# Kernel optimization log

Hardware: AMD Instinct MI355X
Metric: run time of the kernel (lower is better)

## Reference

```python
import jax, jax.numpy as jnp
import numpy as np

NEG_SLOPE = 0.01  # nn.LeakyReLU default


def setup_inputs() -> dict:
    key = jax.random.key(0)
    k1, k2, k3, k4, k5 = jax.random.split(key, 5)
    SLI, FEAT, NODE = 8, 64, 20000
    N = SLI * NODE          # 160000 graph nodes
    E = 2_560_000           # avg degree 16
    OUT = 64
    inputs = jax.random.normal(k1, (SLI, FEAT, NODE), dtype=jnp.float32)
    src = jax.random.randint(k2, (E,), 0, N, dtype=jnp.int64)
    dst = jax.random.randint(k3, (E,), 0, N, dtype=jnp.int64)
    # GraphConv params (glorot-ish scale)
    W = jax.random.normal(k4, (FEAT, OUT), dtype=jnp.float32) / np.sqrt(FEAT)
    b = jnp.zeros((OUT,), dtype=jnp.float32)
    return {"inputs": inputs, "W": W, "b": b, "src": src, "dst": dst}


def reference(inputs, W, b, src, dst):
    # inputs: [sli, feat, node] -> [sli*node, feat]  (dropout is eval-mode identity)
    sli, feat, node = inputs.shape
    x = jnp.transpose(inputs, (0, 2, 1)).reshape(-1, feat)
    N = sli * node
    ones = jnp.ones(src.shape, dtype=x.dtype)
    deg_out = jax.ops.segment_sum(ones, src, num_segments=N)  # out-degree of src
    deg_in = jax.ops.segment_sum(ones, dst, num_segments=N)   # in-degree of dst
    norm_src = jnp.where(deg_out > 0, deg_out, 1.0) ** -0.5
    norm_dst = jnp.where(deg_in > 0, deg_in, 1.0) ** -0.5
    # norm='both': scale src feats, sum-aggregate over edges, scale dst
    h = x * norm_src[:, None]
    agg = jax.ops.segment_sum(h[src], dst, num_segments=N)    # [N, feat]
    agg = agg * norm_dst[:, None]
    out = agg @ W + b                                          # [N, out]
    out = jax.nn.leaky_relu(out, NEG_SLOPE)
    # [N, out] -> [sli, node, out] -> [sli, out, node]
    return jnp.transpose(out.reshape(sli, node, -1), (0, 2, 1))
```

## Files before the change

kernel.cpp:

```cpp
#include <hip/hip_runtime.h>
#include <hip/hip_bf16.h>

constexpr int SLI  = 8;
constexpr int FEAT = 64;
constexpr int NODE = 20000;
constexpr int NTOT = SLI * NODE;
constexpr int OUTF = 64;
constexpr int CAP  = 48;
constexpr int NBD  = 625;
constexpr int NBS  = 313;
constexpr int BCAPD = 4864;
constexpr int BCAPS = 8960;
constexpr int EPB  = 4096;
constexpr int NDST = NTOT / 256;

typedef __attribute__((ext_vector_type(8))) short bf16x8;
typedef __attribute__((ext_vector_type(4))) float f32x4;

static __device__ inline unsigned short f2bf(float x) {
    unsigned u = __float_as_uint(x);
    unsigned r = (u + 0x7fffu + ((u >> 16) & 1u)) >> 16;
    return (unsigned short)r;
}

__global__ __launch_bounds__(256) void k_part(const int* __restrict__ src,
                                              const int* __restrict__ dst,
                                              int* __restrict__ cursor_d,
                                              unsigned* __restrict__ bucket_d,
                                              int* __restrict__ cursor_s,
                                              unsigned short* __restrict__ bucket_s, int E) {
    __shared__ unsigned       svalD[EPB];
    __shared__ unsigned short sbktD[EPB];
    __shared__ unsigned sS[EPB];
    __shared__ int histD[NBD], loffD[NBD], lcurD[NBD], baseD[NBD];
    __shared__ int histS[NBS], loffS[NBS], lcurS[NBS], baseS[NBS];
    __shared__ int goffD[64], goffS[64];
    int t  = threadIdx.x;
    int e0 = blockIdx.x * EPB;
    for (int i = t; i < NBD; i += 256) histD[i] = 0;
    for (int i = t; i < NBS; i += 256) histS[i] = 0;
    __syncthreads();
    int myS[16], myD[16];
#pragma unroll
    for (int i = 0; i < 4; ++i) {
        int j  = (e0 >> 2) + i * 256 + t;
        int b4 = j << 2;
        if (b4 + 3 < E) {
            int4 vs = ((const int4*)src)[j];
            int4 vd = ((const int4*)dst)[j];
            myS[4*i+0] = vs.x; myS[4*i+1] = vs.y; myS[4*i+2] = vs.z; myS[4*i+3] = vs.w;
            myD[4*i+0] = vd.x; myD[4*i+1] = vd.y; myD[4*i+2] = vd.z; myD[4*i+3] = vd.w;
        } else {
#pragma unroll
            for (int c = 0; c < 4; ++c) {
                int idx = b4 + c;
                myS[4*i+c] = (idx < E) ? src[idx] : -1;
                myD[4*i+c] = (idx < E) ? dst[idx] : -1;
            }
        }
    }
#pragma unroll
    for (int i = 0; i < 16; ++i) {
        if (myD[i] >= 0) {
            atomicAdd(&histD[myD[i] >> 8], 1);
            atomicAdd(&histS[myS[i] >> 9], 1);
        }
    }
    __syncthreads();
    int wv = t >> 6, ln = t & 63;
    if (wv == 0) {
        int b0 = ln * 10, s = 0;
#pragma unroll
        for (int j = 0; j < 10; ++j) { int bb = b0 + j; if (bb < NBD) s += histD[bb]; }
        int x = s;
        for (int off = 1; off < 64; off <<= 1) {
            int y = __shfl_up(x, off, 64);
            if (ln >= off) x += y;
        }
        goffD[ln] = x - s;
    } else if (wv == 1) {
        int b0 = ln * 5, s = 0;
#pragma unroll
        for (int j = 0; j < 5; ++j) { int bb = b0 + j; if (bb < NBS) s += histS[bb]; }
        int x = s;
        for (int off = 1; off < 64; off <<= 1) {
            int y = __shfl_up(x, off, 64);
            if (ln >= off) x += y;
        }
        goffS[ln] = x - s;
    }
    __syncthreads();
    for (int bb = t; bb < NBD; bb += 256) {
        int g = bb / 10;
        int sD = goffD[g];
        for (int k = g * 10; k < bb; ++k) sD += histD[k];
        loffD[bb] = sD; lcurD[bb] = sD;
        baseD[bb] = atomicAdd(&cursor_d[bb], histD[bb]);
    }
    for (int bb = t; bb < NBS; bb += 256) {
        int g = bb / 5;
        int sS2 = goffS[g];
        for (int k = g * 5; k < bb; ++k) sS2 += histS[k];
        loffS[bb] = sS2; lcurS[bb] = sS2;
        baseS[bb] = atomicAdd(&cursor_s[bb], histS[bb]);
    }
    __syncthreads();
#pragma unroll
    for (int i = 0; i < 16; ++i) {
        if (myD[i] >= 0) {
            int bD = myD[i] >> 8;
            int p  = atomicAdd(&lcurD[bD], 1);
            svalD[p] = ((unsigned)(myD[i] & 255) << 18) | (unsigned)myS[i];
            sbktD[p] = (unsigned short)bD;
            int bS = myS[i] >> 9;
            int q  = atomicAdd(&lcurS[bS], 1);
            sS[q] = ((unsigned)bS << 9) | (unsigned)(myS[i] & 511);
        }
    }
    __syncthreads();
    int nval = E - e0; if (nval > EPB) nval = EPB;
    for (int p = t; p < nval; p += 256) {
        int bD = sbktD[p];
        int wi = baseD[bD] + (p - loffD[bD]);
        if (wi < BCAPD) bucket_d[(size_t)bD * BCAPD + wi] = svalD[p];
        unsigned vs = sS[p];
        int bS = vs >> 9;
        int wj = baseS[bS] + (p - loffS[bS]);
        if (wj < BCAPS) bucket_s[(size_t)bS * BCAPS + wj] = (unsigned short)(vs & 511);
    }
}

__global__ __launch_bounds__(256) void k_fin(const int* __restrict__ cursor_d,
                                             const unsigned* __restrict__ bucket_d,
                                             const int* __restrict__ cursor_s,
                                             const unsigned short* __restrict__ bucket_s,
                                             int* __restrict__ col_ell,
                                             int* __restrict__ deg_in,
                                             int* __restrict__ deg_out) {
    __shared__ char lds[256 * CAP * 4 + 2048];
    int t = threadIdx.x;
    if (blockIdx.x < NDST) {
        int* ell = (int*)lds;
        int* cnt = (int*)(lds + 256 * CAP * 4);
        int b = blockIdx.x;
        cnt[t] = 0;
        __syncthreads();
        int len = cursor_d[b]; if (len > BCAPD) len = BCAPD;
        const unsigned* p = bucket_d + (size_t)b * BCAPD;
        for (int i = t; i < len; i += 256) {
            unsigned e = p[i];
            int r = (e >> 18) & 255;
            int pos = atomicAdd(&cnt[r], 1);
            if (pos < CAP) ell[r * CAP + pos] = (int)(e & 0x3FFFFu);
        }
        __syncthreads();
        int node0 = b << 8;
        deg_in[node0 + t] = cnt[t];
        size_t gbase = (size_t)node0 * CAP;
        const int4* lsrc = (const int4*)ell;
        int4* gdst = (int4*)(col_ell + gbase);
#pragma unroll
        for (int i = 0; i < 12; ++i)
            gdst[i * 256 + t] = lsrc[i * 256 + t];
    } else {
        int* cnt = (int*)lds;
        int b = blockIdx.x - NDST;
        cnt[t] = 0; cnt[t + 256] = 0;
        __syncthreads();
        int len = cursor_s[b]; if (len > BCAPS) len = BCAPS;
        const unsigned short* p = bucket_s + (size_t)b * BCAPS;
        for (int i = t; i < len; i += 256)
            atomicAdd(&cnt[p[i]], 1);
        __syncthreads();
        int n0 = b << 9;
        if (n0 + t < NTOT)       deg_out[n0 + t] = cnt[t];
        if (n0 + 256 + t < NTOT) deg_out[n0 + 256 + t] = cnt[t + 256];
    }
}

__global__ __launch_bounds__(256) void k_transpose(const float* __restrict__ in,
                                                   const int* __restrict__ deg_out,
                                                   unsigned short* __restrict__ xs) {
    __shared__ float tile[64][65];
    int sli = blockIdx.y;
    int n0  = blockIdx.x * 64;
    int t   = threadIdx.x;
    int fx  = t & 15;
    int fr  = t >> 4;
    const float* ip = in + (size_t)sli * FEAT * NODE;
    int nq = n0 + fx * 4;
#pragma unroll
    for (int i = 0; i < 4; ++i) {
        int f = fr + i * 16;
        float4 v = {0.f, 0.f, 0.f, 0.f};
        if (nq < NODE) v = *(const float4*)(ip + (size_t)f * NODE + nq);
        tile[f][fx * 4 + 0] = v.x;
        tile[f][fx * 4 + 1] = v.y;
        tile[f][fx * 4 + 2] = v.z;
        tile[f][fx * 4 + 3] = v.w;
    }
    __syncthreads();
    int h  = t & 31;
    int nr = t >> 5;
#pragma unroll
    for (int i = 0; i < 8; ++i) {
        int nl   = nr + i * 8;
        int node = n0 + nl;
        if (node < NODE) {
            int n = sli * NODE + node;
            int d = deg_out[n];
            float sc = rsqrtf(d > 0 ? (float)d : 1.f);
            unsigned lo = f2bf(tile[2 * h][nl] * sc);
            unsigned hi = f2bf(tile[2 * h + 1][nl] * sc);
            *(unsigned*)(xs + (size_t)n * 64 + 2 * h) = lo | (hi << 16);
        }
    }
}

__global__ __launch_bounds__(256) void k_agg_gemm(const int* __restrict__ deg_in,
                                                  const int* __restrict__ col_ell,
                                                  const unsigned short* __restrict__ xs,
                                                  const float* __restrict__ W,
                                                  const float* __restrict__ b,
                                                  float* __restrict__ out) {
    __shared__ char lds[18432];
    unsigned short* av = (unsigned short*)lds;
    unsigned short* wt = (unsigned short*)(lds + 9216);
    float (*otile)[65] = (float(*)[65])lds;

    int t    = threadIdx.x;
    int lane = t & 63;
    int w    = t >> 6;
    int g8   = lane >> 3;
    int f8   = lane & 7;
    int sli  = blockIdx.y;
    int n0   = blockIdx.x * 64;

#pragma unroll
    for (int i = 0; i < 16; ++i) {
        int idx = i * 256 + t;
        int f = idx >> 6, o = idx & 63;
        wt[o * 72 + f] = f2bf(W[idx]);
    }

    int m0 = w * 16;
    for (int ii = 0; ii < 16; ii += 2) {
        int rowA = m0 + ii, rowB = rowA + 1;
        int nodeA = n0 + rowA, nodeB = n0 + rowB;
        int nA = sli * NODE + nodeA, nB = sli * NODE + nodeB;
        int dA = (nodeA < NODE) ? deg_in[nA] : 0;
        int dB = (nodeB < NODE) ? deg_in[nB] : 0;
        int degA = dA < CAP ? dA : CAP;
        int degB = dB < CAP ? dB : CAP;
        int cA = (lane < degA) ? col_ell[(size_t)nA * CAP + lane] : NTOT;
        int cB = (lane < degB) ? col_ell[(size_t)nB * CAP + lane] : NTOT;
        float accA[8] = {0,0,0,0,0,0,0,0};
        float accB[8] = {0,0,0,0,0,0,0,0};
        int gmax = degA > degB ? degA : degB;
        int groups = (gmax + 7) >> 3;
#pragma unroll 2
        for (int j = 0; j < groups; ++j) {
            int idx = 8 * j + g8;
            int sA = __shfl(cA, idx, 64);
            int sB = __shfl(cB, idx, 64);
            uint4 vA = *(const uint4*)(xs + (size_t)sA * 64 + f8 * 8);
            uint4 vB = *(const uint4*)(xs + (size_t)sB * 64 + f8 * 8);
            accA[0] += __uint_as_float(vA.x << 16);
            accA[1] += __uint_as_float(vA.x & 0xffff0000u);
            accA[2] += __uint_as_float(vA.y << 16);
            accA[3] += __uint_as_float(vA.y & 0xffff0000u);
            accA[4] += __uint_as_float(vA.z << 16);
            accA[5] += __uint_as_float(vA.z & 0xffff0000u);
            accA[6] += __uint_as_float(vA.w << 16);
            accA[7] += __uint_as_float(vA.w & 0xffff0000u);
            accB[0] += __uint_as_float(vB.x << 16);
            accB[1] += __uint_as_float(vB.x & 0xffff0000u);
            accB[2] += __uint_as_float(vB.y << 16);
            accB[3] += __uint_as_float(vB.y & 0xffff0000u);
            accB[4] += __uint_as_float(vB.z << 16);
            accB[5] += __uint_as_float(vB.z & 0xffff0000u);
            accB[6] += __uint_as_float(vB.w << 16);
            accB[7] += __uint_as_float(vB.w & 0xffff0000u);
        }
#pragma unroll
        for (int k = 0; k < 8; ++k) {
            accA[k] += __shfl_xor(accA[k], 8, 64);
            accA[k] += __shfl_xor(accA[k], 16, 64);
            accA[k] += __shfl_xor(accA[k], 32, 64);
            accB[k] += __shfl_xor(accB[k], 8, 64);
            accB[k] += __shfl_xor(accB[k], 16, 64);
            accB[k] += __shfl_xor(accB[k], 32, 64);
        }
        if (g8 == 0) {
            float scA = rsqrtf(dA > 0 ? (float)dA : 1.f);
            float scB = rsqrtf(dB > 0 ? (float)dB : 1.f);
            uint4 hv;
            hv.x = (unsigned)f2bf(accA[0] * scA) | ((unsigned)f2bf(accA[1] * scA) << 16);
            hv.y = (unsigned)f2bf(accA[2] * scA) | ((unsigned)f2bf(accA[3] * scA) << 16);
            hv.z = (unsigned)f2bf(accA[4] * scA) | ((unsigned)f2bf(accA[5] * scA) << 16);
            hv.w = (unsigned)f2bf(accA[6] * scA) | ((unsigned)f2bf(accA[7] * scA) << 16);
            ((uint4*)(av + rowA * 72))[f8] = hv;
            hv.x = (unsigned)f2bf(accB[0] * scB) | ((unsigned)f2bf(accB[1] * scB) << 16);
            hv.y = (unsigned)f2bf(accB[2] * scB) | ((unsigned)f2bf(accB[3] * scB) << 16);
            hv.z = (unsigned)f2bf(accB[4] * scB) | ((unsigned)f2bf(accB[5] * scB) << 16);
            hv.w = (unsigned)f2bf(accB[6] * scB) | ((unsigned)f2bf(accB[7] * scB) << 16);
            ((uint4*)(av + rowB * 72))[f8] = hv;
        }
    }

    __syncthreads();

    int q = lane >> 4, r16 = lane & 15;
    bf16x8 afr[2], bfr[4][2];
#pragma unroll
    for (int ks = 0; ks < 2; ++ks)
        afr[ks] = *(const bf16x8*)(av + (m0 + r16) * 72 + ks * 32 + q * 8);
#pragma unroll
    for (int nt = 0; nt < 4; ++nt)
#pragma unroll
        for (int ks = 0; ks < 2; ++ks)
            bfr[nt][ks] = *(const bf16x8*)(wt + (nt * 16 + r16) * 72 + ks * 32 + q * 8);

    f32x4 acc4[4];
#pragma unroll
    for (int nt = 0; nt < 4; ++nt) acc4[nt] = (f32x4){0.f, 0.f, 0.f, 0.f};
#pragma unroll
    for (int nt = 0; nt < 4; ++nt)
#pragma unroll
        for (int ks = 0; ks < 2; ++ks)
            acc4[nt] = __builtin_amdgcn_mfma_f32_16x16x32_bf16(afr[ks], bfr[nt][ks], acc4[nt], 0, 0, 0);
    __syncthreads();

#pragma unroll
    for (int nt = 0; nt < 4; ++nt) {
        int oc = nt * 16 + r16;
        float bias = b[oc];
#pragma unroll
        for (int r = 0; r < 4; ++r) {
            float v = acc4[nt][r] + bias;
            v = v > 0.f ? v : 0.01f * v;
            otile[oc][m0 + q * 4 + r] = v;
        }
    }
    __syncthreads();

    const size_t obase = (size_t)sli * OUTF * NODE;
#pragma unroll
    for (int i = 0; i < 16; ++i) {
        int o    = w + i * 4;
        int node = n0 + lane;
        if (node < NODE)
            out[obase + (size_t)o * NODE + node] = otile[o][lane];
    }
}

extern "C" void kernel_launch(void* const* d_in, const int* in_sizes, int n_in,
                              void* d_out, int out_size, void* d_ws, size_t ws_size,
                              hipStream_t stream) {
    const float* inputs = (const float*)d_in[0];
    const float* W      = (const float*)d_in[1];
    const float* b      = (const float*)d_in[2];
    const int*   src    = (const int*)d_in[3];
    const int*   dst    = (const int*)d_in[4];
    float*       out    = (float*)d_out;
    const int E = in_sizes[3];

    char* ws = (char*)d_ws;
    int* deg_out = (int*)ws;
    int* deg_in  = (int*)(ws + (size_t)NTOT * 4);
    int* col_ell = (int*)(ws + (size_t)2 * NTOT * 4);
    char* R      = (char*)col_ell + (size_t)NTOT * CAP * 4;
    unsigned*       bucket_d = (unsigned*)R;
    unsigned short* bucket_s = (unsigned short*)(R + (size_t)NBD * BCAPD * 4);
    int*            cursors  = (int*)(R + (size_t)NBD * BCAPD * 4 + (size_t)NBS * BCAPS * 2);
    int* cursor_d = cursors;
    int* cursor_s = cursors + NBD;
    unsigned short* xs = (unsigned short*)R;

    hipMemsetAsync(cursors, 0, (size_t)(NBD + NBS) * 4, stream);
    hipMemsetAsync(xs + (size_t)NTOT * 64, 0, 64 * sizeof(unsigned short), stream);

    int PB = (E + EPB - 1) / EPB;
    k_part<<<PB, 256, 0, stream>>>(src, dst, cursor_d, bucket_d, cursor_s, bucket_s, E);

    k_fin<<<NDST + NBS, 256, 0, stream>>>(cursor_d, bucket_d, cursor_s, bucket_s,
                                          col_ell, deg_in, deg_out);

    dim3 tgrid((NODE + 63) / 64, SLI);
    k_transpose<<<tgrid, 256, 0, stream>>>(inputs, deg_out, xs);

    k_agg_gemm<<<tgrid, 256, 0, stream>>>(deg_in, col_ell, xs, W, b, out);
}
```

Baseline: 243.5 us.

## Issue partition cursor atomics early and widen finalize kernel to 512 threads

In the partition kernel, the global atomicAdd reservations on the bucket cursors now start right after the histogram, so their latency overlaps the in-block scan and scatter. Full __syncthreads are swapped for LDS-only waitcnt barriers, which do not wait on the pending global atomics. The loff arrays are dropped and recomputed as lcur minus hist, freeing LDS. The finalize kernel runs 512 threads per block for more parallelism per bucket, at the cost of more register pressure and reliance on hand-written barrier asm being correct.

Result: faster. 223.3 us (-8.3%).

```diff
diff --git a/kernel.cpp b/kernel.cpp
--- a/kernel.cpp
+++ b/kernel.cpp
@@ -32,8 +32,8 @@
     __shared__ unsigned       svalD[EPB];
     __shared__ unsigned short sbktD[EPB];
     __shared__ unsigned sS[EPB];
-    __shared__ int histD[NBD], loffD[NBD], lcurD[NBD], baseD[NBD];
-    __shared__ int histS[NBS], loffS[NBS], lcurS[NBS], baseS[NBS];
+    __shared__ int histD[NBD], lcurD[NBD], baseD[NBD];
+    __shared__ int histS[NBS], lcurS[NBS], baseS[NBS];
     __shared__ int goffD[64], goffS[64];
     int t  = threadIdx.x;
     int e0 = blockIdx.x * EPB;
@@ -67,6 +67,17 @@
         }
     }
     __syncthreads();
+    int rbD[3], rbS[2];
+#pragma unroll
+    for (int i = 0; i < 3; ++i) {
+        int bb = t + i * 256;
+        rbD[i] = (bb < NBD) ? atomicAdd(&cursor_d[bb], histD[bb]) : 0;
+    }
+#pragma unroll
+    for (int i = 0; i < 2; ++i) {
+        int bb = t + i * 256;
+        rbS[i] = (bb < NBS) ? atomicAdd(&cursor_s[bb], histS[bb]) : 0;
+    }
     int wv = t >> 6, ln = t & 63;
     if (wv == 0) {
         int b0 = ln * 10, s = 0;
@@ -89,22 +100,20 @@
         }
         goffS[ln] = x - s;
     }
-    __syncthreads();
+    asm volatile("s_waitcnt lgkmcnt(0)\n\ts_barrier" ::: "memory");
     for (int bb = t; bb < NBD; bb += 256) {
         int g = bb / 10;
         int sD = goffD[g];
         for (int k = g * 10; k < bb; ++k) sD += histD[k];
-        loffD[bb] = sD; lcurD[bb] = sD;
-        baseD[bb] = atomicAdd(&cursor_d[bb], histD[bb]);
+        lcurD[bb] = sD;
     }
     for (int bb = t; bb < NBS; bb += 256) {
         int g = bb / 5;
         int sS2 = goffS[g];
         for (int k = g * 5; k < bb; ++k) sS2 += histS[k];
-        loffS[bb] = sS2; lcurS[bb] = sS2;
-        baseS[bb] = atomicAdd(&cursor_s[bb], histS[bb]);
-    }
-    __syncthreads();
+        lcurS[bb] = sS2;
+    }
+    asm volatile("s_waitcnt lgkmcnt(0)\n\ts_barrier" ::: "memory");
 #pragma unroll
     for (int i = 0; i < 16; ++i) {
         if (myD[i] >= 0) {
@@ -117,20 +126,24 @@
             sS[q] = ((unsigned)bS << 9) | (unsigned)(myS[i] & 511);
         }
     }
+#pragma unroll
+    for (int i = 0; i < 3; ++i) { int bb = t + i * 256; if (bb < NBD) baseD[bb] = rbD[i]; }
+#pragma unroll
+    for (int i = 0; i < 2; ++i) { int bb = t + i * 256; if (bb < NBS) baseS[bb] = rbS[i]; }
     __syncthreads();
     int nval = E - e0; if (nval > EPB) nval = EPB;
     for (int p = t; p < nval; p += 256) {
         int bD = sbktD[p];
-        int wi = baseD[bD] + (p - loffD[bD]);
+        int wi = baseD[bD] + (p - (lcurD[bD] - histD[bD]));
         if (wi < BCAPD) bucket_d[(size_t)bD * BCAPD + wi] = svalD[p];
         unsigned vs = sS[p];
         int bS = vs >> 9;
-        int wj = baseS[bS] + (p - loffS[bS]);
+        int wj = baseS[bS] + (p - (lcurS[bS] - histS[bS]));
         if (wj < BCAPS) bucket_s[(size_t)bS * BCAPS + wj] = (unsigned short)(vs & 511);
     }
 }
 
-__global__ __launch_bounds__(256) void k_fin(const int* __restrict__ cursor_d,
+__global__ __launch_bounds__(512) void k_fin(const int* __restrict__ cursor_d,
                                              const unsigned* __restrict__ bucket_d,
                                              const int* __restrict__ cursor_s,
                                              const unsigned short* __restrict__ bucket_s,
@@ -143,11 +156,11 @@
         int* ell = (int*)lds;
         int* cnt = (int*)(lds + 256 * CAP * 4);
         int b = blockIdx.x;
-        cnt[t] = 0;
+        if (t < 256) cnt[t] = 0;
         __syncthreads();
         int len = cursor_d[b]; if (len > BCAPD) len = BCAPD;
         const unsigned* p = bucket_d + (size_t)b * BCAPD;
-        for (int i = t; i < len; i += 256) {
+        for (int i = t; i < len; i += 512) {
             unsigned e = p[i];
             int r = (e >> 18) & 255;
             int pos = atomicAdd(&cnt[r], 1);
@@ -155,26 +168,25 @@
         }
         __syncthreads();
         int node0 = b << 8;
-        deg_in[node0 + t] = cnt[t];
+        if (t < 256) deg_in[node0 + t] = cnt[t];
         size_t gbase = (size_t)node0 * CAP;
         const int4* lsrc = (const int4*)ell;
         int4* gdst = (int4*)(col_ell + gbase);
 #pragma unroll
-        for (int i = 0; i < 12; ++i)
-            gdst[i * 256 + t] = lsrc[i * 256 + t];
+        for (int i = 0; i < 6; ++i)
+            gdst[i * 512 + t] = lsrc[i * 512 + t];
     } else {
         int* cnt = (int*)lds;
         int b = blockIdx.x - NDST;
-        cnt[t] = 0; cnt[t + 256] = 0;
+        cnt[t] = 0;
         __syncthreads();
         int len = cursor_s[b]; if (len > BCAPS) len = BCAPS;
         const unsigned short* p = bucket_s + (size_t)b * BCAPS;
-        for (int i = t; i < len; i += 256)
+        for (int i = t; i < len; i += 512)
             atomicAdd(&cnt[p[i]], 1);
         __syncthreads();
         int n0 = b << 9;
-        if (n0 + t < NTOT)       deg_out[n0 + t] = cnt[t];
-        if (n0 + 256 + t < NTOT) deg_out[n0 + 256 + t] = cnt[t + 256];
+        if (n0 + t < NTOT) deg_out[n0 + t] = cnt[t];
     }
 }
 
@@ -383,7 +395,7 @@
     int PB = (E + EPB - 1) / EPB;
     k_part<<<PB, 256, 0, stream>>>(src, dst, cursor_d, bucket_d, cursor_s, bucket_s, E);
 
-    k_fin<<<NDST + NBS, 256, 0, stream>>>(cursor_d, bucket_d, cursor_s, bucket_s,
+    k_fin<<<NDST + NBS, 512, 0, stream>>>(cursor_d, bucket_d, cursor_s, bucket_s,
                                           col_ell, deg_in, deg_out);
 
     dim3 tgrid((NODE + 63) / 64, SLI);
```
